# Optimization experiments

Hardware: AMD Instinct MI355X
Metric: run time of the kernel (lower is better)

The kernel has to match this reference:

```python
import jax, jax.numpy as jnp
import numpy as np

SIZES = (1, 2, 4, 8)
C_IN = 64
KC = C_IN // 8      # key_channels = out_channels // 8 = 8
VC = C_IN           # value_channels = out_channels = 64
N_STAGES = len(SIZES)


def setup_inputs() -> dict:
    key = jax.random.key(0)
    ks = jax.random.split(key, 16)
    N, C, H, W = 1, C_IN, 64, 64
    inp = {
        "x1": jax.random.normal(ks[0], (N, C, H, W), jnp.float32),
        "x2": jax.random.normal(ks[1], (N, C, H, W), jnp.float32),
        # per-stage 1x1 conv weights (stacked over the 4 PAM stages)
        "Wq": jax.random.normal(ks[2], (N_STAGES, KC, C), jnp.float32) * 0.02,
        "bq": jnp.zeros((N_STAGES, KC), jnp.float32),
        "gammaq": 1.0 + jax.random.normal(ks[3], (N_STAGES, KC), jnp.float32) * 0.02,
        "betaq": jnp.zeros((N_STAGES, KC), jnp.float32),
        "Wk": jax.random.normal(ks[4], (N_STAGES, KC, C), jnp.float32) * 0.02,
        "bk": jnp.zeros((N_STAGES, KC), jnp.float32),
        "gammak": 1.0 + jax.random.normal(ks[5], (N_STAGES, KC), jnp.float32) * 0.02,
        "betak": jnp.zeros((N_STAGES, KC), jnp.float32),
        "Wv": jax.random.normal(ks[6], (N_STAGES, VC, C), jnp.float32) * 0.02,
        "bv": jnp.zeros((N_STAGES, VC), jnp.float32),
        # final 1x1 conv: in = C * n_stages, out = C, no bias
        "Wo": jax.random.normal(ks[7], (C, VC * N_STAGES), jnp.float32) * 0.02,
    }
    return inp


def _pam_block(x, Wq, bq, gq, betq, Wk, bk, gk, betk, Wv, bv, scale):
    # x: [N, C, H, 2W] (two images concatenated along width)
    N, C, H, W2 = x.shape
    w = W2 // 2
    kc = Wq.shape[0]

    def proj(W, b):  # 1x1 conv
        return jnp.einsum('nchw,kc->nkhw', x, W) + b[:, None, None]

    # BatchNorm (inference form: zero running mean / unit variance) folded to affine
    q = gq[:, None, None] * proj(Wq, bq) + betq[:, None, None]
    k = gk[:, None, None] * proj(Wk, bk) + betk[:, None, None]
    v = proj(Wv, bv)

    hl, wl = H // scale, w // scale

    def to_blocks(t):
        ch = t.shape[1]
        # stack left/right halves on a trailing axis: [N, ch, H, w, 2]
        t = jnp.stack([t[..., :w], t[..., w:]], axis=-1)
        # split into scale x scale spatial blocks -> [N, s*s, ch, hl*wl*2]
        t = t.reshape(N, ch, scale, hl, scale, wl, 2)
        t = t.transpose(0, 2, 4, 1, 3, 5, 6)
        return t.reshape(N, scale * scale, ch, hl * wl * 2)

    qb, kb, vb = to_blocks(q), to_blocks(k), to_blocks(v)

    sim = jnp.einsum('nbkp,nbkq->nbpq', qb, kb) * (kc ** -0.5)
    att = jax.nn.softmax(sim, axis=-1)
    # context = V @ att^T : ctx[c,p] = sum_q v[c,q] * att[p,q]
    ctx = jnp.einsum('nbcq,nbpq->nbcp', vb, att)

    Cv = Wv.shape[0]
    ctx = ctx.reshape(N, scale, scale, Cv, hl, wl, 2)
    ctx = ctx.transpose(0, 3, 1, 4, 2, 5, 6).reshape(N, Cv, H, w, 2)
    # re-concatenate the two halves along width -> [N, Cv, H, 2w]
    return jnp.concatenate([ctx[..., 0], ctx[..., 1]], axis=3)


def reference(x1, x2, Wq, bq, gammaq, betaq, Wk, bk, gammak, betak, Wv, bv, Wo):
    h_w = x1.shape[3]
    x = jnp.concatenate([x1, x2], axis=3)  # [N, C, H, 2W]
    priors = [
        _pam_block(x, Wq[i], bq[i], gammaq[i], betaq[i],
                   Wk[i], bk[i], gammak[i], betak[i],
                   Wv[i], bv[i], SIZES[i])
        for i in range(N_STAGES)
    ]
    cat = jnp.concatenate(priors, axis=1)  # [N, 4C, H, 2W]
    out = jnp.einsum('ndhw,od->nohw', cat, Wo)  # final 1x1 conv, no bias
    return out[:, :, :, :h_w], out[:, :, :, h_w:]


if __name__ == '__main__':
    o1, o2 = reference(**setup_inputs())
    print(o1.shape, o2.shape)
```

## Files before the change

### kernel.cpp

```cpp
#include <hip/hip_runtime.h>


typedef _Float16 f16x8 __attribute__((ext_vector_type(8)));
typedef float f32x16 __attribute__((ext_vector_type(16)));
typedef short bf16x8 __attribute__((ext_vector_type(8)));

__device__ __forceinline__ unsigned short f2bf(float f){
    union{float f;unsigned int i;}v; v.f=f;
    unsigned int r = v.i + 0x7fffu + ((v.i>>16)&1u);
    return (unsigned short)(r>>16);
}
__device__ __forceinline__ unsigned short f2h(float f){
    union{_Float16 h; unsigned short u;}v; v.h = (_Float16)f; return v.u;
}
__device__ __forceinline__ unsigned pack2h(float a, float b){
    auto pk = __builtin_amdgcn_cvt_pkrtz(a, b);
    unsigned u; __builtin_memcpy(&u, &pk, 4); return u;
}
__device__ __forceinline__ float exp2fast(float x){ return __builtin_amdgcn_exp2f(x); }
__device__ __forceinline__ int rfl(int x){ return __builtin_amdgcn_readfirstlane(x); }

#define QMUL 0.5100697233f

__global__ __launch_bounds__(256) void proj_all_kernel(
    const float* __restrict__ x1, const float* __restrict__ x2,
    const float* __restrict__ Wq, const float* __restrict__ bq,
    const float* __restrict__ gq, const float* __restrict__ beq,
    const float* __restrict__ Wk, const float* __restrict__ bk,
    const float* __restrict__ gk, const float* __restrict__ bek,
    const float* __restrict__ Wv, const float* __restrict__ bv,
    unsigned short* __restrict__ Qb, unsigned short* __restrict__ Kb,
    unsigned short* __restrict__ Vf)
{
    __shared__ __align__(16) float xs[64][68];
    __shared__ __align__(16) unsigned vqk[64][8];
    __shared__ __align__(16) unsigned short vv[64][64];

    const int wg = blockIdx.x, st = wg >> 8, rr = wg & 255;
    const int chunk = rr >> 1, cgrp = rr & 1;
    const int lgP = 13 - 2*st, Pm1 = (1<<lgP) - 1;
    const int hb = 6 - st, wlm = (1<<hb) - 1;
    const int t = threadIdx.x;
    const int gp0 = chunk*64;
    const int blk = gp0 >> lgP, p0 = gp0 & Pm1;
    const int si = blk >> st, sj = blk & ((1<<st)-1);
    const int hwbase = ((si<<hb)<<6) | (sj<<hb);

    for (int idx = t; idx < 4096; idx += 256) {
        int c = idx >> 6, g = idx & 63;
        int p = p0 + g, half = p & 1, pw = p >> 1;
        int hw = hwbase | ((pw>>hb)<<6) | (pw & wlm);
        xs[g][c] = (half ? x2 : x1)[c*4096 + hw];
    }
    __syncthreads();

    const int px = t & 63, wv = t >> 6;
    float xr[64];
    #pragma unroll
    for (int q4 = 0; q4 < 16; ++q4)
        *(float4*)&xr[q4*4] = *(const float4*)&xs[px][q4*4];

#define VRANGE(LO,HI)                                              \
    for (int ch = (LO); ch < (HI); ++ch) {                         \
        const int cu = rfl(st*64 + ch);                            \
        const float* wp = Wv + cu*64;                              \
        float d = bv[cu];                                          \
        _Pragma("unroll")                                          \
        for (int k = 0; k < 64; ++k) d += wp[k]*xr[k];             \
        vv[ch][px] = f2h(d);                                       \
    }
#define KPROJ(CH,DST)                                              \
    {   const int cu = rfl(st*8 + (CH));                           \
        const float* wp = Wk + cu*64;                              \
        float d = 0.f;                                             \
        _Pragma("unroll")                                          \
        for (int k = 0; k < 64; ++k) d += wp[k]*xr[k];             \
        float gm = gk[cu];                                         \
        (DST) = gm*(d + bk[cu]) + bek[cu]; }

    if (cgrp == 0) {
        if (wv == 0) {
            float qv8[8];
            for (int ch = 0; ch < 8; ++ch) {
                const int cu = rfl(st*8 + ch);
                const float* wp = Wq + cu*64;
                float d = 0.f;
                #pragma unroll
                for (int k = 0; k < 64; ++k) d += wp[k]*xr[k];
                float gm = gq[cu];
                qv8[ch] = (gm*(d + bq[cu]) + beq[cu])*QMUL;
            }
            #pragma unroll
            for (int i = 0; i < 4; ++i) vqk[px][i] = pack2h(qv8[2*i], qv8[2*i+1]);
            float k0v, k1v; KPROJ(0, k0v) KPROJ(1, k1v)
            vqk[px][4] = pack2h(k0v, k1v);
        } else if (wv == 1) {
            float ka, kb2;
            KPROJ(2, ka) KPROJ(3, kb2) vqk[px][5] = pack2h(ka, kb2);
            KPROJ(4, ka) KPROJ(5, kb2) vqk[px][6] = pack2h(ka, kb2);
            KPROJ(6, ka) KPROJ(7, kb2) vqk[px][7] = pack2h(ka, kb2);
            VRANGE(0, 4)
        } else if (wv == 2) { VRANGE(4, 14) }
        else               { VRANGE(14, 24) }
    } else {
        if      (wv == 0) { VRANGE(24, 34) }
        else if (wv == 1) { VRANGE(34, 44) }
        else if (wv == 2) { VRANGE(44, 54) }
        else              { VRANGE(54, 64) }
    }
#undef VRANGE
#undef KPROJ
    __syncthreads();

    unsigned short* Vst = Vf + st*524288 + (blk << (lgP+6));
    if (cgrp == 0) {
        if (t < 64) {
            *(uint4*)(Qb + st*65536 + (gp0 + t)*8) = *(const uint4*)&vqk[t][0];
        } else if (t < 128) {
            int p2 = t - 64;
            *(uint4*)(Kb + st*65536 + (gp0 + p2)*8) = *(const uint4*)&vqk[p2][4];
        }
        if (t < 192) {
            int ch = t >> 3, q = t & 7;
            int kb = q >> 1, lhi = q & 1;
            unsigned short tmp[8];
            #pragma unroll
            for (int u = 0; u < 8; ++u) {
                int s = q*8 + u;
                tmp[u] = vv[ch][((s&1)<<5) | (s>>1)];
            }
            *(uint4*)(Vst + p0*64 + kb*1024 + (lhi*32 + ch)*8) = *(const uint4*)tmp;
        }
    } else {
        for (int task = t; task < 320; task += 256) {
            int ch = 24 + (task >> 3), q = task & 7;
            int kb = q >> 1, lhi = q & 1;
            int b = (ch >= 32) ? 1 : 0, l31 = ch & 31;
            unsigned short tmp[8];
            #pragma unroll
            for (int u = 0; u < 8; ++u) {
                int s = q*8 + u;
                tmp[u] = vv[ch][((s&1)<<5) | (s>>1)];
            }
            *(uint4*)(Vst + p0*64 + kb*1024 + b*512 + (lhi*32 + l31)*8) = *(const uint4*)tmp;
        }
    }
}

template<int NITER>
__device__ __forceinline__ void attn_core(
    const unsigned short* __restrict__ Kg,
    const unsigned short* __restrict__ Vg,
    int kbase, f16x8 qb, int lane, unsigned msk,
    f32x16& acc0, f32x16& acc1, float* rs)
{
    const int l31 = lane & 31;
    for (int it = 0; it < NITER; ++it) {
        const int k0 = kbase + it*64;
        uint4 ku0 = *(const uint4*)(Kg + (k0 + l31)*8);
        uint4 ku1 = *(const uint4*)(Kg + (k0 + 32 + l31)*8);
        ku0.x &= msk; ku0.y &= msk; ku0.z &= msk; ku0.w &= msk;
        ku1.x &= msk; ku1.y &= msk; ku1.z &= msk; ku1.w &= msk;
        f16x8 ka0, ka1;
        __builtin_memcpy(&ka0, &ku0, 16);
        __builtin_memcpy(&ka1, &ku1, 16);

        f32x16 S0, S1;
        #pragma unroll
        for (int r = 0; r < 16; ++r) { S0[r] = 0.f; S1[r] = 0.f; }
        S0 = __builtin_amdgcn_mfma_f32_32x32x16_f16(ka0, qb, S0, 0, 0, 0);
        S1 = __builtin_amdgcn_mfma_f32_32x32x16_f16(ka1, qb, S1, 0, 0, 0);

        unsigned pw[16];
        #pragma unroll
        for (int r = 0; r < 16; ++r) {
            float e0 = exp2fast(S0[r]);
            float e1 = exp2fast(S1[r]);
            rs[r & 3] += e0 + e1;
            pw[r] = pack2h(e0, e1);
        }

        #pragma unroll
        for (int kc = 0; kc < 4; ++kc) {
            f16x8 pb;
            __builtin_memcpy(&pb, &pw[kc*4], 16);
            const unsigned short* vbase = Vg + (k0 + kc*16)*64;
            f16x8 vb0 = *(const f16x8*)(vbase + lane*8);
            f16x8 vb1 = *(const f16x8*)(vbase + 512 + lane*8);
            acc0 = __builtin_amdgcn_mfma_f32_32x32x16_f16(pb, vb0, acc0, 0, 0, 0);
            acc1 = __builtin_amdgcn_mfma_f32_32x32x16_f16(pb, vb1, acc1, 0, 0, 0);
        }
    }
}

__global__ __launch_bounds__(256, 4) void attn_kernel(
    const unsigned short* __restrict__ Qb, const unsigned short* __restrict__ Kb,
    const unsigned short* __restrict__ Vf,
    float* __restrict__ PART, float* __restrict__ LPART)
{
    __shared__ __align__(16) float BB[8192];
    __shared__ float SCm[4][64];

    const int wg = blockIdx.x;
    const int t = threadIdx.x, lane = t & 63, wv = t >> 6;
    const int l31 = lane & 31, lhi = lane >> 5;

    int st, qt, slot, kbase, mode;
    if (wg < 2048)      { st=0; qt=wg>>3; slot=wg&7;
                          kbase=(wg&7)*1024 + wv*256; mode=4; }
    else if (wg < 2560) { int r=wg-2048; st=1; qt=r>>1; slot=8+(r&1);
                          kbase=(r&1)*1024 + wv*256;  mode=4; }
    else if (wg < 2816) { st=2; qt=wg-2560; slot=10; kbase=wv*128; mode=2; }
    else                { st=3; qt=wg-2816; slot=11; kbase=wv*64;
                          mode=(wv<2)?1:0; }

    const int lgP = 13 - 2*st, P = 1 << lgP;
    const int blk = qt >> (lgP - 5);
    const int q0  = (qt & ((P>>5)-1)) * 32;

    const unsigned short* Qg = Qb + st*65536 + blk*P*8;
    const unsigned short* Kg = Kb + st*65536 + blk*P*8;
    const unsigned short* Vg = Vf + st*524288 + blk*P*64;

    f16x8 qb = *(const f16x8*)(Qg + (q0 + l31)*8);
    const unsigned msk = (lane < 32) ? 0xFFFFFFFFu : 0u;

    f32x16 acc0, acc1;
    #pragma unroll
    for (int r = 0; r < 16; ++r) { acc0[r] = 0.f; acc1[r] = 0.f; }
    float rs[4] = {0.f, 0.f, 0.f, 0.f};

    if      (mode == 4) attn_core<4>(Kg, Vg, kbase, qb, lane, msk, acc0, acc1, rs);
    else if (mode == 2) attn_core<2>(Kg, Vg, kbase, qb, lane, msk, acc0, acc1, rs);
    else if (mode == 1) attn_core<1>(Kg, Vg, kbase, qb, lane, msk, acc0, acc1, rs);

    SCm[wv][lane] = rs[0] + rs[1] + rs[2] + rs[3];
    {
        float* B = BB + wv*2048;
        #pragma unroll
        for (int r = 0; r < 16; ++r) {
            int qrow = (r&3) + 8*(r>>2) + 4*lhi;
            B[qrow*64 + l31]      = acc0[r];
            B[qrow*64 + 32 + l31] = acc1[r];
        }
    }
    __syncthreads();

    float4* Pslab4 = (float4*)(PART + slot*524288 + qt*2048);
    const float4* B4 = (const float4*)BB;
    #pragma unroll
    for (int r = 0; r < 2; ++r) {
        int idx = t + r*256;
        float4 a = B4[idx], b = B4[idx+512], c = B4[idx+1024], d = B4[idx+1536];
        Pslab4[idx] = float4{a.x+b.x+c.x+d.x, a.y+b.y+c.y+d.y,
                             a.z+b.z+c.z+d.z, a.w+b.w+c.w+d.w};
    }
    if (t < 32)
        LPART[slot*8192 + qt*32 + t] =
            (SCm[0][t] + SCm[0][32+t]) + (SCm[1][t] + SCm[1][32+t])
          + (SCm[2][t] + SCm[2][32+t]) + (SCm[3][t] + SCm[3][32+t]);
}

__global__ __launch_bounds__(256) void normconv_kernel(
    const float* __restrict__ PART, const float* __restrict__ LPART,
    const float* __restrict__ Wo, float* __restrict__ out)
{
    __shared__ __align__(16) unsigned short csb[32][264];
    __shared__ __align__(16) unsigned short wof[16384];
    __shared__ float voutf[64][33];
    __shared__ float linv[4][32];
    __shared__ int gpar[4][32];
    const int t = threadIdx.x;
    const int px0 = blockIdx.x * 32;

    {
        int oc = t >> 2, d0 = (t & 3) * 64;
        for (int b = 0; b < 8; ++b) {
            int d = d0 + b*8;
            float4 w0 = *(const float4*)(Wo + oc*256 + d);
            float4 w1 = *(const float4*)(Wo + oc*256 + d + 4);
            unsigned short tmp[8];
            tmp[0]=f2bf(w0.x); tmp[1]=f2bf(w0.y); tmp[2]=f2bf(w0.z); tmp[3]=f2bf(w0.w);
            tmp[4]=f2bf(w1.x); tmp[5]=f2bf(w1.y); tmp[6]=f2bf(w1.z); tmp[7]=f2bf(w1.w);
            *(uint4*)&wof[(d>>3)*512 + oc*8] = *(const uint4*)tmp;
        }
    }
    if (t < 128) {
        const int s0tab[4] = {0,8,10,11};
        const int sctab[4] = {8,2,1,1};
        int stt = t >> 5, i = t & 31;
        int pix = px0 + i;
        int half = pix >> 12, hw = pix & 4095;
        int h = hw >> 6, w = hw & 63;
        int hb = 6 - stt, wlm = (1<<hb)-1;
        int si = h >> hb, sj = w >> hb, hi = h & wlm, wi = w & wlm;
        int blk = (si << stt) | sj;
        int p = (((hi << hb) | wi) << 1) | half;
        int gp = blk*(8192>>(2*stt)) + p;
        gpar[stt][i] = gp;
        int s0 = s0tab[stt];
        float l = LPART[s0*8192 + gp];
        for (int c = 1; c < sctab[stt]; ++c) l += LPART[(s0+c)*8192 + gp];
        linv[stt][i] = 1.f / l;
    }
    __syncthreads();

    {
        const int s0tab[4] = {0,8,10,11};
        const int sctab[4] = {8,2,1,1};
        int gpx = t >> 3, cvg = (t & 7) * 8;
        for (int stt = 0; stt < 4; ++stt) {
            int gp = gpar[stt][gpx];
            const float* p = PART + s0tab[stt]*524288
                           + (gp>>5)*2048 + (gp&31)*64 + cvg;
            float4 a = *(const float4*)p;
            float4 b = *(const float4*)(p + 4);
            for (int c = 1; c < sctab[stt]; ++c) {
                float4 a2 = *(const float4*)(p + c*524288);
                float4 b2 = *(const float4*)(p + c*524288 + 4);
                a.x+=a2.x; a.y+=a2.y; a.z+=a2.z; a.w+=a2.w;
                b.x+=b2.x; b.y+=b2.y; b.z+=b2.z; b.w+=b2.w;
            }
            float li = linv[stt][gpx];
            unsigned short tmp[8];
            tmp[0]=f2bf(a.x*li); tmp[1]=f2bf(a.y*li); tmp[2]=f2bf(a.z*li); tmp[3]=f2bf(a.w*li);
            tmp[4]=f2bf(b.x*li); tmp[5]=f2bf(b.y*li); tmp[6]=f2bf(b.z*li); tmp[7]=f2bf(b.w*li);
            *(uint4*)&csb[gpx][stt*64 + cvg] = *(const uint4*)tmp;
        }
    }
    __syncthreads();

    const int lane = t & 63, wvv = t >> 6;
    const int l31 = lane & 31, lhi = lane >> 5;
    const int nh = wvv & 1, kh = wvv >> 1;
    f32x16 acc;
    #pragma unroll
    for (int r = 0; r < 16; ++r) acc[r] = 0.f;
    #pragma unroll
    for (int s = 0; s < 8; ++s) {
        int dg = kh*16 + s*2 + lhi;
        bf16x8 a = *(const bf16x8*)&csb[l31][kh*128 + s*16 + 8*lhi];
        bf16x8 b = *(const bf16x8*)&wof[dg*512 + (nh*32 + l31)*8];
        acc = __builtin_amdgcn_mfma_f32_32x32x16_bf16(a, b, acc, 0, 0, 0);
    }
    if (kh == 0) {
        #pragma unroll
        for (int r = 0; r < 16; ++r)
            voutf[nh*32 + l31][(r&3) + 8*(r>>2) + 4*lhi] = acc[r];
    }
    __syncthreads();
    if (kh == 1) {
        #pragma unroll
        for (int r = 0; r < 16; ++r)
            voutf[nh*32 + l31][(r&3) + 8*(r>>2) + 4*lhi] += acc[r];
    }
    __syncthreads();

    const int half = px0 >> 12, hw0 = px0 & 4095;
    float* obase = out + half*262144 + hw0;
    #pragma unroll
    for (int r = 0; r < 8; ++r) {
        int idx = t + r*256;
        int oc = idx >> 5, pxi = idx & 31;
        obase[oc*4096 + pxi] = voutf[oc][pxi];
    }
}

extern "C" void kernel_launch(void* const* d_in, const int* in_sizes, int n_in,
                              void* d_out, int out_size, void* d_ws, size_t ws_size,
                              hipStream_t stream)
{
    (void)out_size; (void)ws_size;
    const float *x1, *x2, *Wq, *bq, *gq, *beq, *Wk, *bk, *gk, *bek, *Wv, *bv, *Wo;

    if (n_in >= 13 && in_sizes[0] == 2048) {
        Wk  = (const float*)d_in[0];  Wo  = (const float*)d_in[1];
        Wq  = (const float*)d_in[2];  Wv  = (const float*)d_in[3];
        bek = (const float*)d_in[4];  beq = (const float*)d_in[5];
        bk  = (const float*)d_in[6];  bq  = (const float*)d_in[7];
        bv  = (const float*)d_in[8];  gk  = (const float*)d_in[9];
        gq  = (const float*)d_in[10];
        x1  = (const float*)d_in[11]; x2  = (const float*)d_in[12];
    } else {
        x1  = (const float*)d_in[0];  x2  = (const float*)d_in[1];
        Wq  = (const float*)d_in[2];  bq  = (const float*)d_in[3];
        gq  = (const float*)d_in[4];  beq = (const float*)d_in[5];
        Wk  = (const float*)d_in[6];  bk  = (const float*)d_in[7];
        gk  = (const float*)d_in[8];  bek = (const float*)d_in[9];
        Wv  = (const float*)d_in[10]; bv  = (const float*)d_in[11];
        Wo  = (const float*)d_in[12];
    }

    unsigned short* Qb = (unsigned short*)d_ws;
    unsigned short* Kb = Qb + 262144;
    unsigned short* Vf = Kb + 262144;
    float* PART  = (float*)d_ws + 1310720;
    float* LPART = PART + 6291456;

    proj_all_kernel<<<1024, 256, 0, stream>>>(x1,x2,Wq,bq,gq,beq,Wk,bk,gk,bek,Wv,bv,Qb,Kb,Vf);
    attn_kernel<<<3072, 256, 0, stream>>>(Qb,Kb,Vf,PART,LPART);
    normconv_kernel<<<256, 256, 0, stream>>>(PART, LPART, Wo, (float*)d_out);
}
```

Before: 133.5 us.

## Give each wave its own query tile and partial slot, drop LDS reduction

The attention work split changes so that each wave in a workgroup handles an independent query tile and key split and writes its own partial accumulator slot straight to global memory. This removes the LDS staging buffer, the __syncthreads and the in-block four-way reduction, and it shrinks the grid from 3072 to 1728 workgroups. In exchange the partial buffer grows (27 slots instead of 12), so the attention kernel writes and normconv reads more partial data, with up to 16 slots summed per pixel for stage 0. The per-lane scattered float stores are also less coalesced than the previous float4 stores.

```diff
diff --git a/kernel.cpp b/kernel.cpp
--- a/kernel.cpp
+++ b/kernel.cpp
@@ -198,21 +198,30 @@
     const unsigned short* __restrict__ Vf,
     float* __restrict__ PART, float* __restrict__ LPART)
 {
-    __shared__ __align__(16) float BB[8192];
-    __shared__ float SCm[4][64];
-
     const int wg = blockIdx.x;
     const int t = threadIdx.x, lane = t & 63, wv = t >> 6;
     const int l31 = lane & 31, lhi = lane >> 5;
 
     int st, qt, slot, kbase, mode;
-    if (wg < 2048)      { st=0; qt=wg>>3; slot=wg&7;
-                          kbase=(wg&7)*1024 + wv*256; mode=4; }
-    else if (wg < 2560) { int r=wg-2048; st=1; qt=r>>1; slot=8+(r&1);
-                          kbase=(r&1)*1024 + wv*256;  mode=4; }
-    else if (wg < 2816) { st=2; qt=wg-2560; slot=10; kbase=wv*128; mode=2; }
-    else                { st=3; qt=wg-2816; slot=11; kbase=wv*64;
-                          mode=(wv<2)?1:0; }
+    if (wg < 1024) {
+        st = 0; int tp = wg >> 3, sp = wg & 7;
+        qt = tp*2 + (wv & 1);
+        int ls = sp*2 + (wv >> 1);
+        slot = ls; kbase = ls*512; mode = 8;
+    } else if (wg < 1536) {
+        st = 1; int r = wg - 1024; int tp = r >> 2, sp = r & 3;
+        qt = tp*2 + (wv & 1);
+        int ls = sp*2 + (wv >> 1);
+        slot = 16 + ls; kbase = ls*256; mode = 4;
+    } else if (wg < 1664) {
+        st = 2; int r = wg - 1536;
+        qt = r*2 + (wv & 1);
+        int ls = (wv >> 1);
+        slot = 24 + ls; kbase = ls*256; mode = 4;
+    } else {
+        st = 3; int r = wg - 1664;
+        qt = r*4 + wv; slot = 26; kbase = 0; mode = 2;
+    }
 
     const int lgP = 13 - 2*st, P = 1 << lgP;
     const int blk = qt >> (lgP - 5);
@@ -230,35 +239,22 @@
     for (int r = 0; r < 16; ++r) { acc0[r] = 0.f; acc1[r] = 0.f; }
     float rs[4] = {0.f, 0.f, 0.f, 0.f};
 
-    if      (mode == 4) attn_core<4>(Kg, Vg, kbase, qb, lane, msk, acc0, acc1, rs);
-    else if (mode == 2) attn_core<2>(Kg, Vg, kbase, qb, lane, msk, acc0, acc1, rs);
-    else if (mode == 1) attn_core<1>(Kg, Vg, kbase, qb, lane, msk, acc0, acc1, rs);
-
-    SCm[wv][lane] = rs[0] + rs[1] + rs[2] + rs[3];
-    {
-        float* B = BB + wv*2048;
-        #pragma unroll
-        for (int r = 0; r < 16; ++r) {
-            int qrow = (r&3) + 8*(r>>2) + 4*lhi;
-            B[qrow*64 + l31]      = acc0[r];
-            B[qrow*64 + 32 + l31] = acc1[r];
-        }
-    }
-    __syncthreads();
-
-    float4* Pslab4 = (float4*)(PART + slot*524288 + qt*2048);
-    const float4* B4 = (const float4*)BB;
-    #pragma unroll
-    for (int r = 0; r < 2; ++r) {
-        int idx = t + r*256;
-        float4 a = B4[idx], b = B4[idx+512], c = B4[idx+1024], d = B4[idx+1536];
-        Pslab4[idx] = float4{a.x+b.x+c.x+d.x, a.y+b.y+c.y+d.y,
-                             a.z+b.z+c.z+d.z, a.w+b.w+c.w+d.w};
-    }
-    if (t < 32)
-        LPART[slot*8192 + qt*32 + t] =
-            (SCm[0][t] + SCm[0][32+t]) + (SCm[1][t] + SCm[1][32+t])
-          + (SCm[2][t] + SCm[2][32+t]) + (SCm[3][t] + SCm[3][32+t]);
+    if      (mode == 8) attn_core<8>(Kg, Vg, kbase, qb, lane, msk, acc0, acc1, rs);
+    else if (mode == 4) attn_core<4>(Kg, Vg, kbase, qb, lane, msk, acc0, acc1, rs);
+    else                attn_core<2>(Kg, Vg, kbase, qb, lane, msk, acc0, acc1, rs);
+
+    float lsum = rs[0] + rs[1] + rs[2] + rs[3];
+    lsum += __shfl_xor(lsum, 32);
+
+    float* Pw = PART + slot*524288 + qt*2048;
+    #pragma unroll
+    for (int r = 0; r < 16; ++r) {
+        int qrow = (r&3) + 8*(r>>2) + 4*lhi;
+        Pw[qrow*64 + l31]      = acc0[r];
+        Pw[qrow*64 + 32 + l31] = acc1[r];
+    }
+    if (lane < 32)
+        LPART[slot*8192 + qt*32 + l31] = lsum;
 }
 
 __global__ __launch_bounds__(256) void normconv_kernel(
@@ -286,8 +282,8 @@
         }
     }
     if (t < 128) {
-        const int s0tab[4] = {0,8,10,11};
-        const int sctab[4] = {8,2,1,1};
+        const int s0tab[4] = {0,16,24,26};
+        const int sctab[4] = {16,8,2,1};
         int stt = t >> 5, i = t & 31;
         int pix = px0 + i;
         int half = pix >> 12, hw = pix & 4095;
@@ -306,8 +302,8 @@
     __syncthreads();
 
     {
-        const int s0tab[4] = {0,8,10,11};
-        const int sctab[4] = {8,2,1,1};
+        const int s0tab[4] = {0,16,24,26};
+        const int sctab[4] = {16,8,2,1};
         int gpx = t >> 3, cvg = (t & 7) * 8;
         for (int stt = 0; stt < 4; ++stt) {
             int gp = gpar[stt][gpx];
@@ -395,9 +391,9 @@
     unsigned short* Kb = Qb + 262144;
     unsigned short* Vf = Kb + 262144;
     float* PART  = (float*)d_ws + 1310720;
-    float* LPART = PART + 6291456;
+    float* LPART = PART + 14155776;
 
     proj_all_kernel<<<1024, 256, 0, stream>>>(x1,x2,Wq,bq,gq,beq,Wk,bk,gk,bek,Wv,bv,Qb,Kb,Vf);
-    attn_kernel<<<3072, 256, 0, stream>>>(Qb,Kb,Vf,PART,LPART);
+    attn_kernel<<<1728, 256, 0, stream>>>(Qb,Kb,Vf,PART,LPART);
     normconv_kernel<<<256, 256, 0, stream>>>(PART, LPART, Wo, (float*)d_out);
 }
```

Result: slower. 136.7 us (+2.4%).
